# Kernel tuning notes

Measured on AMD Instinct MI355X. Metric: run time of the kernel, lower is better.

The kernel has to match this reference:

```python
import jax, jax.numpy as jnp
import numpy as np

NUM_EXPERTS = 8
TOP_K = 2

def setup_inputs() -> dict:
    key = jax.random.key(0)
    ks = jax.random.split(key, 5)
    B, S, D, F, E = 4, 2048, 1024, 4096, NUM_EXPERTS
    x = jax.random.normal(ks[0], (B, S, D), dtype=jnp.float32)
    router_w = jax.random.normal(ks[1], (D, E), dtype=jnp.float32) * 0.02
    router_b = jnp.zeros((E,), dtype=jnp.float32)
    w1 = jax.random.normal(ks[2], (E, D, F), dtype=jnp.float32) * 0.02
    b1 = jnp.zeros((E, F), dtype=jnp.float32)
    w2 = jax.random.normal(ks[3], (E, F, D), dtype=jnp.float32) * 0.02
    b2 = jnp.zeros((E, D), dtype=jnp.float32)
    return {"x": x, "router_w": router_w, "router_b": router_b,
            "w1": w1, "b1": b1, "w2": w2, "b2": b2}

def reference(x, router_w, router_b, w1, b1, w2, b2):
    B, S, D = x.shape
    E = router_w.shape[1]
    x_flat = x.reshape(-1, D)                                  # [N, D]
    router_probs = jax.nn.softmax(x_flat @ router_w + router_b, axis=-1)  # [N, E]
    topk_probs, topk_idx = jax.lax.top_k(router_probs, TOP_K)  # [N, K]
    topk_probs = topk_probs / jnp.sum(topk_probs, axis=-1, keepdims=True)
    # combine weight per (token, expert): sum over top-k slots assigned to that expert
    cw = jnp.sum(topk_probs[..., None] * jax.nn.one_hot(topk_idx, E, dtype=x.dtype), axis=1)  # [N, E]
    out = jnp.zeros_like(x_flat)
    for e in range(E):  # small fixed expert count; each iter is a dense GEMM pair
        h = jax.nn.gelu(x_flat @ w1[e] + b1[e], approximate=False)  # [N, F]
        out = out + cw[:, e:e + 1] * (h @ w2[e] + b2[e])            # [N, D]
    return out.reshape(B, S, D)
```

## Files before the change

### kernel.cpp

```cpp
#include <hip/hip_runtime.h>
#include <hip/hip_bf16.h>

typedef __attribute__((ext_vector_type(8))) __bf16 bf16x8;
typedef __attribute__((ext_vector_type(4))) float f32x4;

#define NTOK 8192
#define D_DIM 1024
#define F_DIM 4096
#define NEXP 8
#define SLOT_TOT 16384
#define SLOT_CAP 16640
#define TILE_MAX 136

__device__ __forceinline__ unsigned short f2b(float f) {
  __hip_bfloat16 b = __float2bfloat16(f);
  return reinterpret_cast<unsigned short&>(b);
}

__device__ __forceinline__ float gelu_f(float v) {
  const float y2 = v * (1.5957691216f + 0.0713548162f * v * v);
  return v * __builtin_amdgcn_rcpf(1.f + __expf(-y2));
}

__device__ __forceinline__ void gload_lds16(const void* g, void* l) {
  __builtin_amdgcn_global_load_lds(
      (__attribute__((address_space(1))) void*)g,
      (__attribute__((address_space(3))) void*)l, 16, 0, 0);
}


__global__ void init_counts_kernel(int* counts) {
  if (threadIdx.x < NEXP) counts[threadIdx.x] = 0;
}

__global__ void zero_out_kernel(float* out) {
  const int i = blockIdx.x * 256 + threadIdx.x;
  reinterpret_cast<float4*>(out)[i] = make_float4(0.f, 0.f, 0.f, 0.f);
}

__global__ void scatter_gather_kernel(const float* __restrict__ x,
                                      const int* __restrict__ topk_idx,
                                      int* __restrict__ cursors,
                                      int* __restrict__ slot_pos,
                                      __hip_bfloat16* __restrict__ xg) {
  __shared__ int ps[2];
  const int tok = blockIdx.x;
  const int tid = threadIdx.x;
  if (tid < 2) {
    const int e = topk_idx[tok * 2 + tid];
    const int p = atomicAdd(&cursors[e], 1);
    slot_pos[tok * 2 + tid] = p;
    ps[tid] = p;
  }
  __syncthreads();
  const int d = tid * 4;
  const float4 v = *reinterpret_cast<const float4*>(x + (size_t)tok * D_DIM + d);
  union { unsigned short u[4]; uint2 q; } o;
  o.u[0] = f2b(v.x); o.u[1] = f2b(v.y); o.u[2] = f2b(v.z); o.u[3] = f2b(v.w);
  *reinterpret_cast<uint2*>(xg + (size_t)ps[0] * D_DIM + d) = o.q;
  *reinterpret_cast<uint2*>(xg + (size_t)ps[1] * D_DIM + d) = o.q;
}

__global__ void combine_kernel(const __hip_bfloat16* __restrict__ ys,
                               const int* __restrict__ slot_pos,
                               const float* __restrict__ topk_w,
                               float* __restrict__ out) {
  const int tok = blockIdx.x;
  const int d = threadIdx.x * 4;
  const int s0 = slot_pos[tok * 2], s1 = slot_pos[tok * 2 + 1];
  const float w0 = topk_w[tok * 2], w1 = topk_w[tok * 2 + 1];
  union { unsigned short u[4]; uint2 q; } a, b;
  a.q = *reinterpret_cast<const uint2*>(ys + (size_t)s0 * D_DIM + d);
  b.q = *reinterpret_cast<const uint2*>(ys + (size_t)s1 * D_DIM + d);
  float4 rr;
  float va[4];
  #pragma unroll
  for (int i = 0; i < 4; ++i) {
    unsigned int ua = (unsigned int)a.u[i] << 16;
    unsigned int ub = (unsigned int)b.u[i] << 16;
    va[i] = w0 * reinterpret_cast<float&>(ua) + w1 * reinterpret_cast<float&>(ub);
  }
  rr.x = va[0]; rr.y = va[1]; rr.z = va[2]; rr.w = va[3];
  *reinterpret_cast<float4*>(out + (size_t)tok * D_DIM + d) = rr;
}

__global__ void transpose_conv_kernel(const float* __restrict__ src,
                                      __hip_bfloat16* __restrict__ dst,
                                      int R, int C) {
  __shared__ float tile[64][65];
  const int e = blockIdx.z;
  src += (size_t)e * R * C;
  dst += (size_t)e * R * C;
  const int c0 = blockIdx.x * 64, r0 = blockIdx.y * 64;
  const int tx = threadIdx.x, ty = threadIdx.y;
  #pragma unroll
  for (int j = 0; j < 4; ++j) {
    const float4 v = *reinterpret_cast<const float4*>(
        &src[(size_t)(r0 + ty + j * 16) * C + c0 + tx * 4]);
    tile[ty + j * 16][tx * 4 + 0] = v.x;
    tile[ty + j * 16][tx * 4 + 1] = v.y;
    tile[ty + j * 16][tx * 4 + 2] = v.z;
    tile[ty + j * 16][tx * 4 + 3] = v.w;
  }
  __syncthreads();
  #pragma unroll
  for (int j = 0; j < 4; ++j) {
    const int c = ty + j * 16;
    union { unsigned short u[4]; uint2 d; } o;
    #pragma unroll
    for (int i = 0; i < 4; ++i) o.u[i] = f2b(tile[tx * 4 + i][c]);
    *reinterpret_cast<uint2*>(&dst[(size_t)(c0 + c) * R + r0 + tx * 4]) = o.d;
  }
}

__global__ void router_kernel(const float* __restrict__ x,
                              const float* __restrict__ rw,
                              const float* __restrict__ rb,
                              int* __restrict__ topk_idx,
                              float* __restrict__ topk_w,
                              int* __restrict__ counts) {
  __shared__ float rwT[NEXP * D_DIM];
  const int tid = threadIdx.x;
  for (int i = tid; i < NEXP * D_DIM; i += 256) {
    const int d = i >> 3, e = i & 7;
    rwT[e * D_DIM + d] = rw[i];
  }
  __syncthreads();

  const int wave = tid >> 6, lane = tid & 63;
  const int tok = blockIdx.x * 4 + wave;
  const float* xr = x + (size_t)tok * D_DIM;

  float acc[NEXP];
  #pragma unroll
  for (int e = 0; e < NEXP; ++e) acc[e] = 0.f;

  for (int i = 0; i < D_DIM / 64; ++i) {
    const int d = i * 64 + lane;
    const float xv = xr[d];
    #pragma unroll
    for (int e = 0; e < NEXP; ++e) acc[e] += xv * rwT[e * D_DIM + d];
  }
  #pragma unroll
  for (int off = 32; off > 0; off >>= 1) {
    #pragma unroll
    for (int e = 0; e < NEXP; ++e) acc[e] += __shfl_xor(acc[e], off);
  }

  if (lane == 0) {
    float l[NEXP];
    #pragma unroll
    for (int e = 0; e < NEXP; ++e) l[e] = acc[e] + rb[e];
    int i1 = 0;
    #pragma unroll
    for (int e = 1; e < NEXP; ++e) if (l[e] > l[i1]) i1 = e;
    int i2 = (i1 == 0) ? 1 : 0;
    #pragma unroll
    for (int e = 0; e < NEXP; ++e) if (e != i1 && e != i2 && l[e] > l[i2]) i2 = e;
    const float w1 = 1.f / (1.f + __expf(l[i2] - l[i1]));
    topk_idx[tok * 2 + 0] = i1;
    topk_idx[tok * 2 + 1] = i2;
    topk_w[tok * 2 + 0] = w1;
    topk_w[tok * 2 + 1] = 1.f - w1;
    atomicAdd(&counts[i1], 1);
    atomicAdd(&counts[i2], 1);
  }
}

__global__ void offsets_kernel(const int* __restrict__ counts,
                               int* __restrict__ offsets,
                               int* __restrict__ cursors,
                               int* __restrict__ tile_meta) {
  if (threadIdx.x == 0) {
    int s = 0;
    for (int e = 0; e < NEXP; ++e) { offsets[e] = s; cursors[e] = s; s += counts[e]; }
    offsets[NEXP] = s;
    int n = 0;
    for (int e = 0; e < NEXP; ++e) {
      const int ntile = (counts[e] + 127) >> 7;
      for (int m = 0; m < ntile && n < TILE_MAX; ++m) tile_meta[n++] = e | (m << 8);
    }
    for (; n < TILE_MAX; ++n) tile_meta[n] = 0 | (1 << 22);
  }
}

template <int PHASE>
__global__ __launch_bounds__(256, 4) void moe_gemm(
    const __hip_bfloat16* __restrict__ A,
    const __hip_bfloat16* __restrict__ B,
    const float* __restrict__ bias,
    const int* __restrict__ counts,
    const int* __restrict__ offsets,
    const int* __restrict__ tile_meta,
    __hip_bfloat16* __restrict__ Cout) {
  constexpr int K    = (PHASE == 1) ? D_DIM : F_DIM;
  constexpr int NCOL = (PHASE == 1) ? F_DIM : D_DIM;
  constexpr int NT   = NCOL / 128;
  constexpr int KT   = K / 32;

  const int bid = blockIdx.x;
  const int j = bid / NT, nt = bid % NT;
  const int meta = tile_meta[j];
  const int e = meta & 255, mt = meta >> 8;
  const int cnt = counts[e];
  if (mt * 128 >= cnt) return;
  const int base = offsets[e];

  __shared__ unsigned short lds[2][8192];

  const int tid = threadIdx.x;
  const int w = tid >> 6, lane = tid & 63;
  const int r = lane & 15, kg = lane >> 4;
  const int wm = w >> 1, wn = w & 1;

  const __hip_bfloat16* gA0 = A + (size_t)(base + mt * 128 + w * 16 + r) * K + kg * 8;
  const __hip_bfloat16* gA1 = gA0 + (size_t)64 * K;
  const __hip_bfloat16* gB0 = B + ((size_t)e * NCOL + nt * 128 + w * 16 + r) * K + kg * 8;
  const __hip_bfloat16* gB1 = gB0 + (size_t)64 * K;

  f32x4 acc[4][4] = {};

  auto stage = [&](unsigned short* buf) {
    gload_lds16(gA0, buf + w * 512);
    gload_lds16(gA1, buf + (w + 4) * 512);
    gload_lds16(gB0, buf + 4096 + w * 512);
    gload_lds16(gB1, buf + 4096 + (w + 4) * 512);
    gA0 += 32; gA1 += 32; gB0 += 32; gB1 += 32;
  };
  auto compute = [&](const unsigned short* buf) {
    bf16x8 af[4], bfr[4];
    #pragma unroll
    for (int i2 = 0; i2 < 4; ++i2) {
      af[i2]  = *(const bf16x8*)(buf + (wm * 4 + i2) * 512 + lane * 8);
      bfr[i2] = *(const bf16x8*)(buf + 4096 + (wn * 4 + i2) * 512 + lane * 8);
    }
    #pragma unroll
    for (int mi = 0; mi < 4; ++mi)
      #pragma unroll
      for (int ni = 0; ni < 4; ++ni)
        acc[mi][ni] = __builtin_amdgcn_mfma_f32_16x16x32_bf16(
            af[mi], bfr[ni], acc[mi][ni], 0, 0, 0);
  };

  unsigned short* pc = lds[0];
  unsigned short* pn = lds[1];

  stage(pc);
  __syncthreads();
  for (int t = 0; t < KT - 1; ++t) {
    stage(pn);
    compute(pc);
    __syncthreads();
    unsigned short* ts = pc; pc = pn; pn = ts;
  }
  compute(pc);

  const int rem = cnt - mt * 128;
  const int q4 = (lane >> 4) * 4;
  const int c15 = lane & 15;

  if (rem >= 128) {
    #pragma unroll
    for (int n = 0; n < 4; ++n) {
      const int col = nt * 128 + wn * 64 + n * 16 + c15;
      const float bv = bias[e * NCOL + col];
      #pragma unroll
      for (int m = 0; m < 4; ++m) {
        #pragma unroll
        for (int rr = 0; rr < 4; ++rr) {
          const int rloc = wm * 64 + m * 16 + q4 + rr;
          float v = acc[m][n][rr] + bv;
          if constexpr (PHASE == 1) v = gelu_f(v);
          Cout[(size_t)(base + mt * 128 + rloc) * NCOL + col] = __float2bfloat16(v);
        }
      }
    }
  } else {
    #pragma unroll
    for (int n = 0; n < 4; ++n) {
      const int col = nt * 128 + wn * 64 + n * 16 + c15;
      const float bv = bias[e * NCOL + col];
      #pragma unroll
      for (int m = 0; m < 4; ++m) {
        #pragma unroll
        for (int rr = 0; rr < 4; ++rr) {
          const int rloc = wm * 64 + m * 16 + q4 + rr;
          if (rloc < rem) {
            float v = acc[m][n][rr] + bv;
            if constexpr (PHASE == 1) v = gelu_f(v);
            Cout[(size_t)(base + mt * 128 + rloc) * NCOL + col] = __float2bfloat16(v);
          }
        }
      }
    }
  }
}


extern "C" void kernel_launch(void* const* d_in, const int* in_sizes, int n_in,
                              void* d_out, int out_size, void* d_ws, size_t ws_size,
                              hipStream_t stream) {
  const float* x  = (const float*)d_in[0];
  const float* rw = (const float*)d_in[1];
  const float* rb = (const float*)d_in[2];
  const float* w1 = (const float*)d_in[3];
  const float* b1 = (const float*)d_in[4];
  const float* w2 = (const float*)d_in[5];
  const float* b2 = (const float*)d_in[6];
  float* out = (float*)d_out;

  char* p = (char*)d_ws;
  size_t used = 0;
  auto carve = [&](size_t bytes) {
    char* r = p + used;
    used += (bytes + 255) & ~(size_t)255;
    return (void*)r;
  };
  __hip_bfloat16* xg  = (__hip_bfloat16*)carve((size_t)SLOT_CAP * D_DIM * 2);
  __hip_bfloat16* ys  = xg;
  __hip_bfloat16* w1t = (__hip_bfloat16*)carve((size_t)NEXP * F_DIM * D_DIM * 2);
  __hip_bfloat16* w2t = (__hip_bfloat16*)carve((size_t)NEXP * D_DIM * F_DIM * 2);
  __hip_bfloat16* h   = (__hip_bfloat16*)carve((size_t)SLOT_CAP * F_DIM * 2);
  int*   topk_idx   = (int*)carve((size_t)NTOK * 2 * 4);
  float* topk_w     = (float*)carve((size_t)NTOK * 2 * 4);
  int*   slot_pos   = (int*)carve((size_t)NTOK * 2 * 4);
  int*   tile_meta  = (int*)carve(TILE_MAX * 4);
  int* counts  = (int*)carve(256);
  int* offsets = (int*)carve(256);
  int* cursors = (int*)carve(256);

  if (used > ws_size) {
    zero_out_kernel<<<8192, 256, 0, stream>>>(out);
    return;
  }

  init_counts_kernel<<<1, 64, 0, stream>>>(counts);
  router_kernel<<<NTOK / 4, 256, 0, stream>>>(x, rw, rb, topk_idx, topk_w, counts);
  offsets_kernel<<<1, 64, 0, stream>>>(counts, offsets, cursors, tile_meta);
  scatter_gather_kernel<<<NTOK, 256, 0, stream>>>(x, topk_idx, cursors, slot_pos, xg);

  dim3 tb(16, 16);
  transpose_conv_kernel<<<dim3(F_DIM / 64, D_DIM / 64, NEXP), tb, 0, stream>>>(w1, w1t, D_DIM, F_DIM);
  transpose_conv_kernel<<<dim3(D_DIM / 64, F_DIM / 64, NEXP), tb, 0, stream>>>(w2, w2t, F_DIM, D_DIM);

  moe_gemm<1><<<TILE_MAX * (F_DIM / 128), 256, 0, stream>>>(
      xg, w1t, b1, counts, offsets, tile_meta, h);
  moe_gemm<2><<<TILE_MAX * (D_DIM / 128), 256, 0, stream>>>(
      h, w2t, b2, counts, offsets, tile_meta, ys);

  combine_kernel<<<NTOK, 256, 0, stream>>>(ys, slot_pos, topk_w, out);
}
```

Baseline: 986.2 us.

## Use 256x256 tiles with 512 threads for first expert GEMM, widen transpose stores

The first expert GEMM (D→F with GELU) moves to a dedicated kernel that uses 256x256 output tiles, 8 waves, 64-wide K stages and a separate tile list keyed on 256-row blocks. The goal is higher arithmetic intensity and less redundant A/B traffic per FLOP. The cost is 128KB of LDS and a larger register footprint, which limits occupancy to about two blocks per CU, and more padded work on partial expert tiles. The weight transpose kernel is also rewritten to use 1D 256-thread blocks and 16-byte bf16 stores.

```diff
diff --git a/kernel.cpp b/kernel.cpp
--- a/kernel.cpp
+++ b/kernel.cpp
@@ -11,6 +11,7 @@
 #define SLOT_TOT 16384
 #define SLOT_CAP 16640
 #define TILE_MAX 136
+#define TILE_MAX2 72
 
 __device__ __forceinline__ unsigned short f2b(float f) {
   __hip_bfloat16 b = __float2bfloat16(f);
@@ -92,24 +93,25 @@
   src += (size_t)e * R * C;
   dst += (size_t)e * R * C;
   const int c0 = blockIdx.x * 64, r0 = blockIdx.y * 64;
-  const int tx = threadIdx.x, ty = threadIdx.y;
+  const int tid = threadIdx.x;
+  const int lr = tid >> 4, lc4 = (tid & 15) * 4;
   #pragma unroll
-  for (int j = 0; j < 4; ++j) {
+  for (int pass = 0; pass < 4; ++pass) {
+    const int rr = pass * 16 + lr;
     const float4 v = *reinterpret_cast<const float4*>(
-        &src[(size_t)(r0 + ty + j * 16) * C + c0 + tx * 4]);
-    tile[ty + j * 16][tx * 4 + 0] = v.x;
-    tile[ty + j * 16][tx * 4 + 1] = v.y;
-    tile[ty + j * 16][tx * 4 + 2] = v.z;
-    tile[ty + j * 16][tx * 4 + 3] = v.w;
+        &src[(size_t)(r0 + rr) * C + c0 + lc4]);
+    tile[rr][lc4 + 0] = v.x; tile[rr][lc4 + 1] = v.y;
+    tile[rr][lc4 + 2] = v.z; tile[rr][lc4 + 3] = v.w;
   }
   __syncthreads();
+  const int sc = tid >> 3, sr8 = (tid & 7) * 8;
   #pragma unroll
-  for (int j = 0; j < 4; ++j) {
-    const int c = ty + j * 16;
-    union { unsigned short u[4]; uint2 d; } o;
-    #pragma unroll
-    for (int i = 0; i < 4; ++i) o.u[i] = f2b(tile[tx * 4 + i][c]);
-    *reinterpret_cast<uint2*>(&dst[(size_t)(c0 + c) * R + r0 + tx * 4]) = o.d;
+  for (int pass = 0; pass < 2; ++pass) {
+    const int c = pass * 32 + sc;
+    union { unsigned short u[8]; uint4 q; } o;
+    #pragma unroll
+    for (int i = 0; i < 8; ++i) o.u[i] = f2b(tile[sr8 + i][c]);
+    *reinterpret_cast<uint4*>(&dst[(size_t)(c0 + c) * R + r0 + sr8]) = o.q;
   }
 }
 
@@ -170,22 +172,140 @@
 __global__ void offsets_kernel(const int* __restrict__ counts,
                                int* __restrict__ offsets,
                                int* __restrict__ cursors,
-                               int* __restrict__ tile_meta) {
+                               int* __restrict__ tile_meta,
+                               int* __restrict__ tile_meta2) {
   if (threadIdx.x == 0) {
     int s = 0;
     for (int e = 0; e < NEXP; ++e) { offsets[e] = s; cursors[e] = s; s += counts[e]; }
     offsets[NEXP] = s;
     int n = 0;
     for (int e = 0; e < NEXP; ++e) {
-      const int ntile = (counts[e] + 127) >> 7;
-      for (int m = 0; m < ntile && n < TILE_MAX; ++m) tile_meta[n++] = e | (m << 8);
+      const int nt = (counts[e] + 127) >> 7;
+      for (int m = 0; m < nt && n < TILE_MAX; ++m) tile_meta[n++] = e | (m << 8);
     }
     for (; n < TILE_MAX; ++n) tile_meta[n] = 0 | (1 << 22);
-  }
-}
-
-template <int PHASE>
-__global__ __launch_bounds__(256, 4) void moe_gemm(
+    n = 0;
+    for (int e = 0; e < NEXP; ++e) {
+      const int nt = (counts[e] + 255) >> 8;
+      for (int m = 0; m < nt && n < TILE_MAX2; ++m) tile_meta2[n++] = e | (m << 8);
+    }
+    for (; n < TILE_MAX2; ++n) tile_meta2[n] = 0 | (1 << 22);
+  }
+}
+
+__global__ __launch_bounds__(512, 2) void moe_gemm1(
+    const __hip_bfloat16* __restrict__ A,
+    const __hip_bfloat16* __restrict__ B,
+    const float* __restrict__ bias,
+    const int* __restrict__ counts,
+    const int* __restrict__ offsets,
+    const int* __restrict__ tile_meta2,
+    __hip_bfloat16* __restrict__ Hout) {
+  constexpr int K = D_DIM, NCOL = F_DIM;
+  constexpr int KT = K / 64;
+
+  const int bid = blockIdx.x;
+  const int j = bid >> 4, nt = bid & 15;
+  const int meta = tile_meta2[j];
+  const int e = meta & 255, mt = meta >> 8;
+  const int cnt = counts[e];
+  if (mt * 256 >= cnt) return;
+  const int base = offsets[e];
+
+  __shared__ unsigned short lds[2][32768];
+
+  const int tid = threadIdx.x;
+  const int w = tid >> 6, lane = tid & 63;
+  const int r = lane & 15, kg = lane >> 4;
+  const int wm = w >> 2, wn = w & 3;
+
+  const __hip_bfloat16* gA0 = A + (size_t)(base + mt * 256 + w * 16 + r) * K + kg * 8;
+  const __hip_bfloat16* gA1 = gA0 + (size_t)128 * K;
+  const __hip_bfloat16* gB0 = B + ((size_t)e * NCOL + nt * 256 + w * 16 + r) * K + kg * 8;
+  const __hip_bfloat16* gB1 = gB0 + (size_t)128 * K;
+
+  f32x4 acc[8][4] = {};
+
+  auto stage = [&](unsigned short* buf) {
+    gload_lds16(gA0,      buf + w * 512);
+    gload_lds16(gA1,      buf + (w + 8) * 512);
+    gload_lds16(gA0 + 32, buf + (16 + w) * 512);
+    gload_lds16(gA1 + 32, buf + (16 + w + 8) * 512);
+    gload_lds16(gB0,      buf + 16384 + w * 512);
+    gload_lds16(gB1,      buf + 16384 + (w + 8) * 512);
+    gload_lds16(gB0 + 32, buf + 16384 + (16 + w) * 512);
+    gload_lds16(gB1 + 32, buf + 16384 + (16 + w + 8) * 512);
+    gA0 += 64; gA1 += 64; gB0 += 64; gB1 += 64;
+  };
+  auto compute = [&](const unsigned short* buf) {
+    #pragma unroll
+    for (int kk = 0; kk < 2; ++kk) {
+      bf16x8 af[8], bfr[4];
+      #pragma unroll
+      for (int m = 0; m < 8; ++m)
+        af[m] = *(const bf16x8*)(buf + (kk * 16 + wm * 8 + m) * 512 + lane * 8);
+      #pragma unroll
+      for (int n = 0; n < 4; ++n)
+        bfr[n] = *(const bf16x8*)(buf + 16384 + (kk * 16 + wn * 4 + n) * 512 + lane * 8);
+      #pragma unroll
+      for (int m = 0; m < 8; ++m)
+        #pragma unroll
+        for (int n = 0; n < 4; ++n)
+          acc[m][n] = __builtin_amdgcn_mfma_f32_16x16x32_bf16(
+              af[m], bfr[n], acc[m][n], 0, 0, 0);
+    }
+  };
+
+  unsigned short* pc = lds[0];
+  unsigned short* pn = lds[1];
+
+  stage(pc);
+  __syncthreads();
+  for (int t = 0; t < KT - 1; ++t) {
+    stage(pn);
+    compute(pc);
+    __syncthreads();
+    unsigned short* ts = pc; pc = pn; pn = ts;
+  }
+  compute(pc);
+
+  const int rem = cnt - mt * 256;
+  const int q4 = (lane >> 4) * 4;
+  const int c15 = lane & 15;
+
+  if (rem >= 256) {
+    #pragma unroll
+    for (int n = 0; n < 4; ++n) {
+      const int col = nt * 256 + wn * 64 + n * 16 + c15;
+      const float bv = bias[e * NCOL + col];
+      #pragma unroll
+      for (int m = 0; m < 8; ++m)
+        #pragma unroll
+        for (int rr = 0; rr < 4; ++rr) {
+          const int rloc = wm * 128 + m * 16 + q4 + rr;
+          Hout[(size_t)(base + mt * 256 + rloc) * NCOL + col] =
+              __float2bfloat16(gelu_f(acc[m][n][rr] + bv));
+        }
+    }
+  } else {
+    #pragma unroll
+    for (int n = 0; n < 4; ++n) {
+      const int col = nt * 256 + wn * 64 + n * 16 + c15;
+      const float bv = bias[e * NCOL + col];
+      #pragma unroll
+      for (int m = 0; m < 8; ++m)
+        #pragma unroll
+        for (int rr = 0; rr < 4; ++rr) {
+          const int rloc = wm * 128 + m * 16 + q4 + rr;
+          if (rloc < rem)
+            Hout[(size_t)(base + mt * 256 + rloc) * NCOL + col] =
+                __float2bfloat16(gelu_f(acc[m][n][rr] + bv));
+        }
+    }
+  }
+}
+
+__global__ __launch_bounds__(256, 4) void moe_gemm2(
     const __hip_bfloat16* __restrict__ A,
     const __hip_bfloat16* __restrict__ B,
     const float* __restrict__ bias,
@@ -193,10 +313,9 @@
     const int* __restrict__ offsets,
     const int* __restrict__ tile_meta,
     __hip_bfloat16* __restrict__ Cout) {
-  constexpr int K    = (PHASE == 1) ? D_DIM : F_DIM;
-  constexpr int NCOL = (PHASE == 1) ? F_DIM : D_DIM;
-  constexpr int NT   = NCOL / 128;
-  constexpr int KT   = K / 32;
+  constexpr int K = F_DIM, NCOL = D_DIM;
+  constexpr int NT = NCOL / 128;
+  constexpr int KT = K / 32;
 
   const int bid = blockIdx.x;
   const int j = bid / NT, nt = bid % NT;
@@ -265,15 +384,13 @@
       const int col = nt * 128 + wn * 64 + n * 16 + c15;
       const float bv = bias[e * NCOL + col];
       #pragma unroll
-      for (int m = 0; m < 4; ++m) {
+      for (int m = 0; m < 4; ++m)
         #pragma unroll
         for (int rr = 0; rr < 4; ++rr) {
           const int rloc = wm * 64 + m * 16 + q4 + rr;
-          float v = acc[m][n][rr] + bv;
-          if constexpr (PHASE == 1) v = gelu_f(v);
-          Cout[(size_t)(base + mt * 128 + rloc) * NCOL + col] = __float2bfloat16(v);
+          Cout[(size_t)(base + mt * 128 + rloc) * NCOL + col] =
+              __float2bfloat16(acc[m][n][rr] + bv);
         }
-      }
     }
   } else {
     #pragma unroll
@@ -281,17 +398,14 @@
       const int col = nt * 128 + wn * 64 + n * 16 + c15;
       const float bv = bias[e * NCOL + col];
       #pragma unroll
-      for (int m = 0; m < 4; ++m) {
+      for (int m = 0; m < 4; ++m)
         #pragma unroll
         for (int rr = 0; rr < 4; ++rr) {
           const int rloc = wm * 64 + m * 16 + q4 + rr;
-          if (rloc < rem) {
-            float v = acc[m][n][rr] + bv;
-            if constexpr (PHASE == 1) v = gelu_f(v);
-            Cout[(size_t)(base + mt * 128 + rloc) * NCOL + col] = __float2bfloat16(v);
-          }
+          if (rloc < rem)
+            Cout[(size_t)(base + mt * 128 + rloc) * NCOL + col] =
+                __float2bfloat16(acc[m][n][rr] + bv);
         }
-      }
     }
   }
 }
@@ -325,6 +439,7 @@
   float* topk_w     = (float*)carve((size_t)NTOK * 2 * 4);
   int*   slot_pos   = (int*)carve((size_t)NTOK * 2 * 4);
   int*   tile_meta  = (int*)carve(TILE_MAX * 4);
+  int*   tile_meta2 = (int*)carve(TILE_MAX2 * 4);
   int* counts  = (int*)carve(256);
   int* offsets = (int*)carve(256);
   int* cursors = (int*)carve(256);
@@ -336,16 +451,17 @@
 
   init_counts_kernel<<<1, 64, 0, stream>>>(counts);
   router_kernel<<<NTOK / 4, 256, 0, stream>>>(x, rw, rb, topk_idx, topk_w, counts);
-  offsets_kernel<<<1, 64, 0, stream>>>(counts, offsets, cursors, tile_meta);
+  offsets_kernel<<<1, 64, 0, stream>>>(counts, offsets, cursors, tile_meta, tile_meta2);
   scatter_gather_kernel<<<NTOK, 256, 0, stream>>>(x, topk_idx, cursors, slot_pos, xg);
 
-  dim3 tb(16, 16);
-  transpose_conv_kernel<<<dim3(F_DIM / 64, D_DIM / 64, NEXP), tb, 0, stream>>>(w1, w1t, D_DIM, F_DIM);
-  transpose_conv_kernel<<<dim3(D_DIM / 64, F_DIM / 64, NEXP), tb, 0, stream>>>(w2, w2t, F_DIM, D_DIM);
-
-  moe_gemm<1><<<TILE_MAX * (F_DIM / 128), 256, 0, stream>>>(
-      xg, w1t, b1, counts, offsets, tile_meta, h);
-  moe_gemm<2><<<TILE_MAX * (D_DIM / 128), 256, 0, stream>>>(
+  transpose_conv_kernel<<<dim3(F_DIM / 64, D_DIM / 64, NEXP), 256, 0, stream>>>(
+      w1, w1t, D_DIM, F_DIM);
+  transpose_conv_kernel<<<dim3(D_DIM / 64, F_DIM / 64, NEXP), 256, 0, stream>>>(
+      w2, w2t, F_DIM, D_DIM);
+
+  moe_gemm1<<<TILE_MAX2 * (F_DIM / 256), 512, 0, stream>>>(
+      xg, w1t, b1, counts, offsets, tile_meta2, h);
+  moe_gemm2<<<TILE_MAX * (D_DIM / 128), 256, 0, stream>>>(
       h, w2t, b2, counts, offsets, tile_meta, ys);
 
   combine_kernel<<<NTOK, 256, 0, stream>>>(ys, slot_pos, topk_w, out);
```

New measurement: 961.7 us. 1.03x faster.

## Enlarge MoE GEMM tiles to 128x256 with 8 waves and XCD-aware block mapping

Applied to the files above, without the earlier changes.

The expert GEMM block grows from 256 to 512 threads and its tile from 128x128 to 128x256 output columns, so each A tile staged in LDS feeds twice as many columns. Block indices are remapped so consecutive tile rows land on the same XCD, aiming for better L2 reuse of A and B. The weight transpose-convert kernel moves to a 1D 256-thread block and writes 16-byte stores instead of 8-byte ones. Larger LDS use (48KB per block) and 512-thread blocks may reduce occupancy, and the launch bound of 512x4 waves per EU may not be achievable.

```diff
diff --git a/kernel.cpp b/kernel.cpp
--- a/kernel.cpp
+++ b/kernel.cpp
@@ -92,24 +92,25 @@
   src += (size_t)e * R * C;
   dst += (size_t)e * R * C;
   const int c0 = blockIdx.x * 64, r0 = blockIdx.y * 64;
-  const int tx = threadIdx.x, ty = threadIdx.y;
-  #pragma unroll
-  for (int j = 0; j < 4; ++j) {
+  const int tid = threadIdx.x;
+  const int lr = tid >> 4, lc4 = (tid & 15) * 4;
+  #pragma unroll
+  for (int pass = 0; pass < 4; ++pass) {
+    const int rr = pass * 16 + lr;
     const float4 v = *reinterpret_cast<const float4*>(
-        &src[(size_t)(r0 + ty + j * 16) * C + c0 + tx * 4]);
-    tile[ty + j * 16][tx * 4 + 0] = v.x;
-    tile[ty + j * 16][tx * 4 + 1] = v.y;
-    tile[ty + j * 16][tx * 4 + 2] = v.z;
-    tile[ty + j * 16][tx * 4 + 3] = v.w;
+        &src[(size_t)(r0 + rr) * C + c0 + lc4]);
+    tile[rr][lc4 + 0] = v.x; tile[rr][lc4 + 1] = v.y;
+    tile[rr][lc4 + 2] = v.z; tile[rr][lc4 + 3] = v.w;
   }
   __syncthreads();
-  #pragma unroll
-  for (int j = 0; j < 4; ++j) {
-    const int c = ty + j * 16;
-    union { unsigned short u[4]; uint2 d; } o;
-    #pragma unroll
-    for (int i = 0; i < 4; ++i) o.u[i] = f2b(tile[tx * 4 + i][c]);
-    *reinterpret_cast<uint2*>(&dst[(size_t)(c0 + c) * R + r0 + tx * 4]) = o.d;
+  const int sc = tid >> 3, sr8 = (tid & 7) * 8;
+  #pragma unroll
+  for (int pass = 0; pass < 2; ++pass) {
+    const int c = pass * 32 + sc;
+    union { unsigned short u[8]; uint4 q; } o;
+    #pragma unroll
+    for (int i = 0; i < 8; ++i) o.u[i] = f2b(tile[sr8 + i][c]);
+    *reinterpret_cast<uint4*>(&dst[(size_t)(c0 + c) * R + r0 + sr8]) = o.q;
   }
 }
 
@@ -185,7 +186,7 @@
 }
 
 template <int PHASE>
-__global__ __launch_bounds__(256, 4) void moe_gemm(
+__global__ __launch_bounds__(512, 4) void moe_gemm(
     const __hip_bfloat16* __restrict__ A,
     const __hip_bfloat16* __restrict__ B,
     const float* __restrict__ bias,
@@ -195,37 +196,37 @@
     __hip_bfloat16* __restrict__ Cout) {
   constexpr int K    = (PHASE == 1) ? D_DIM : F_DIM;
   constexpr int NCOL = (PHASE == 1) ? F_DIM : D_DIM;
-  constexpr int NT   = NCOL / 128;
+  constexpr int NTSH = (PHASE == 1) ? 4 : 2;
   constexpr int KT   = K / 32;
 
-  const int bid = blockIdx.x;
-  const int j = bid / NT, nt = bid % NT;
+  const int xcd = blockIdx.x & 7;
+  const int local = blockIdx.x >> 3;
+  const int j = xcd * (TILE_MAX / 8) + (local >> NTSH);
+  const int nt = local & ((1 << NTSH) - 1);
   const int meta = tile_meta[j];
   const int e = meta & 255, mt = meta >> 8;
   const int cnt = counts[e];
   if (mt * 128 >= cnt) return;
   const int base = offsets[e];
 
-  __shared__ unsigned short lds[2][8192];
+  __shared__ unsigned short lds[2][12288];
 
   const int tid = threadIdx.x;
   const int w = tid >> 6, lane = tid & 63;
   const int r = lane & 15, kg = lane >> 4;
-  const int wm = w >> 1, wn = w & 1;
+  const int wm = w >> 2, wn = w & 3;
 
   const __hip_bfloat16* gA0 = A + (size_t)(base + mt * 128 + w * 16 + r) * K + kg * 8;
-  const __hip_bfloat16* gA1 = gA0 + (size_t)64 * K;
-  const __hip_bfloat16* gB0 = B + ((size_t)e * NCOL + nt * 128 + w * 16 + r) * K + kg * 8;
-  const __hip_bfloat16* gB1 = gB0 + (size_t)64 * K;
+  const __hip_bfloat16* gB0 = B + ((size_t)e * NCOL + nt * 256 + w * 16 + r) * K + kg * 8;
+  const __hip_bfloat16* gB1 = gB0 + (size_t)128 * K;
 
   f32x4 acc[4][4] = {};
 
   auto stage = [&](unsigned short* buf) {
     gload_lds16(gA0, buf + w * 512);
-    gload_lds16(gA1, buf + (w + 4) * 512);
     gload_lds16(gB0, buf + 4096 + w * 512);
-    gload_lds16(gB1, buf + 4096 + (w + 4) * 512);
-    gA0 += 32; gA1 += 32; gB0 += 32; gB1 += 32;
+    gload_lds16(gB1, buf + 4096 + (w + 8) * 512);
+    gA0 += 32; gB0 += 32; gB1 += 32;
   };
   auto compute = [&](const unsigned short* buf) {
     bf16x8 af[4], bfr[4];
@@ -262,7 +263,7 @@
   if (rem >= 128) {
     #pragma unroll
     for (int n = 0; n < 4; ++n) {
-      const int col = nt * 128 + wn * 64 + n * 16 + c15;
+      const int col = nt * 256 + wn * 64 + n * 16 + c15;
       const float bv = bias[e * NCOL + col];
       #pragma unroll
       for (int m = 0; m < 4; ++m) {
@@ -278,7 +279,7 @@
   } else {
     #pragma unroll
     for (int n = 0; n < 4; ++n) {
-      const int col = nt * 128 + wn * 64 + n * 16 + c15;
+      const int col = nt * 256 + wn * 64 + n * 16 + c15;
       const float bv = bias[e * NCOL + col];
       #pragma unroll
       for (int m = 0; m < 4; ++m) {
@@ -339,13 +340,14 @@
   offsets_kernel<<<1, 64, 0, stream>>>(counts, offsets, cursors, tile_meta);
   scatter_gather_kernel<<<NTOK, 256, 0, stream>>>(x, topk_idx, cursors, slot_pos, xg);
 
-  dim3 tb(16, 16);
-  transpose_conv_kernel<<<dim3(F_DIM / 64, D_DIM / 64, NEXP), tb, 0, stream>>>(w1, w1t, D_DIM, F_DIM);
-  transpose_conv_kernel<<<dim3(D_DIM / 64, F_DIM / 64, NEXP), tb, 0, stream>>>(w2, w2t, F_DIM, D_DIM);
-
-  moe_gemm<1><<<TILE_MAX * (F_DIM / 128), 256, 0, stream>>>(
+  transpose_conv_kernel<<<dim3(F_DIM / 64, D_DIM / 64, NEXP), 256, 0, stream>>>(
+      w1, w1t, D_DIM, F_DIM);
+  transpose_conv_kernel<<<dim3(D_DIM / 64, F_DIM / 64, NEXP), 256, 0, stream>>>(
+      w2, w2t, F_DIM, D_DIM);
+
+  moe_gemm<1><<<TILE_MAX * (F_DIM / 256), 512, 0, stream>>>(
       xg, w1t, b1, counts, offsets, tile_meta, h);
-  moe_gemm<2><<<TILE_MAX * (D_DIM / 128), 256, 0, stream>>>(
+  moe_gemm<2><<<TILE_MAX * (D_DIM / 256), 512, 0, stream>>>(
       h, w2t, b2, counts, offsets, tile_meta, ys);
 
   combine_kernel<<<NTOK, 256, 0, stream>>>(ys, slot_pos, topk_w, out);
```

New measurement: 975.3 us. About the same (-1.1%).
